# Kernel optimization log

Measured on AMD Instinct MI355X. Metric: run time of the kernel, lower is better.

## Reference

```python
import jax, jax.numpy as jnp
import numpy as np

FACTOR = 5

def setup_inputs() -> dict:
    key = jax.random.key(0)
    kq, kk, kv, ki = jax.random.split(key, 4)
    B, L, H, D = 8, 2048, 8, 64
    u = FACTOR * int(np.ceil(np.log(L)))  # sample_k == n_top == 40
    return {
        "queries": jax.random.normal(kq, (B, L, H, D), dtype=jnp.float32),
        "keys": jax.random.normal(kk, (B, L, H, D), dtype=jnp.float32),
        "values": jax.random.normal(kv, (B, L, H, D), dtype=jnp.float32),
        "index_sample": jax.random.randint(ki, (L, u), 0, L, dtype=jnp.int32),
    }

def reference(queries, keys, values, index_sample):
    B, L, H, D = queries.shape
    # faithful to torch .view(B, H, -1, D) on contiguous tensors (a reshape, not a transpose)
    q = queries.reshape(B, H, L, D)
    k = keys.reshape(B, H, L, D)
    v = values.reshape(B, H, L, D)
    u = FACTOR * int(np.ceil(np.log(L)))  # U_part == u
    # --- _prob_QK: sample keys per query, score, pick top-u queries ---
    K_sample = k[:, :, index_sample, :]                      # [B,H,L,u,D] gather over L_K
    QK_sample = jnp.einsum('bhld,bhlsd->bhls', q, K_sample)  # [B,H,L,u]
    M = QK_sample.max(axis=-1) - QK_sample.sum(axis=-1) / L  # sparsity measure [B,H,L]
    M_top = jax.lax.top_k(M, u)[1]                           # [B,H,u] indices of active queries
    Q_reduce = jnp.take_along_axis(q, M_top[..., None], axis=2)  # [B,H,u,D]
    scores = jnp.einsum('bhud,bhld->bhul', Q_reduce, k)      # [B,H,u,L]
    scale = 1.0 / float(np.sqrt(D))
    attn = jax.nn.softmax(scores * scale, axis=-1)           # dropout is identity in eval
    context = jnp.einsum('bhul,bhld->bhud', attn, v)         # [B,H,u,D]
    return context, attn
```

## Files before the change

### kernel.cpp

```cpp
#include <hip/hip_runtime.h>
#include <math.h>

#define LSEQ 2048
#define DDIM 64
#define UU   40
#define NBH  64
#define NCHUNK 8
#define CROWS  256
#define CTX_ELEMS (NBH*UU*DDIM)

__device__ __forceinline__ float grp8_sum(float x) {
  float t;
  t = __int_as_float(__builtin_amdgcn_update_dpp(0, __float_as_int(x), 0xB1, 0xF, 0xF, false));
  x += t;
  t = __int_as_float(__builtin_amdgcn_update_dpp(0, __float_as_int(x), 0x4E, 0xF, 0xF, false));
  x += t;
  t = __int_as_float(__builtin_amdgcn_update_dpp(0, __float_as_int(x), 0x141, 0xF, 0xF, false));
  x += t;
  return x;
}

__global__ __launch_bounds__(256) void k0_sort(
    const int* __restrict__ idxs, int* __restrict__ sidx, int* __restrict__ soff) {
  int l = blockIdx.x * 4 + (threadIdx.x >> 6);
  int lane = threadIdx.x & 63;
  int v = 0, c = NCHUNK;
  if (lane < UU) { v = idxs[l * UU + lane]; c = v >> 8; }
  unsigned long long lower = (1ull << lane) - 1ull;
  int base = 0;
#pragma unroll
  for (int cc = 0; cc < NCHUNK; ++cc) {
    unsigned long long m = __ballot(c == cc);
    if (c == cc) {
      int rank = __popcll(m & lower);
      sidx[l * UU + base + rank] = v;
    }
    int cnt = __popcll(m);
    if (lane == cc) soff[l * NCHUNK + cc] = (base << 8) | cnt;
    base += cnt;
  }
}

__global__ __launch_bounds__(512, 4) void k12_gather(
    const float* __restrict__ q, const float* __restrict__ k,
    const int* __restrict__ sidx, const int* __restrict__ soff,
    float2* __restrict__ Mpart) {
  __shared__ float4 kt[CROWS * 16];
  int b = blockIdx.x;
  int bh = b & 63;
  int c  = b >> 6;
  int t  = threadIdx.x;

  {
    const float4* src = (const float4*)(k + ((size_t)bh * LSEQ + c * CROWS) * DDIM);
#pragma unroll
    for (int j = 0; j < 8; ++j) {
      int i = t + 512 * j;
      int row = i >> 4, col = i & 15;
      kt[row * 16 + (col ^ (row & 7))] = src[i];
    }
  }
  __syncthreads();

  int w = t >> 6;
  int lane = t & 63;
  int g = lane >> 3;
  int sub = lane & 7;

  for (int lb = 0; lb < 256; lb += 8) {
    int l = w * 256 + lb + g;
    const float4* qr = (const float4*)(q + ((size_t)bh * LSEQ + l) * DDIM);
    float4 qa = qr[sub];
    float4 qb = qr[sub + 8];
    int oc   = soff[l * NCHUNK + c];
    int cnt  = oc & 255;
    int base = oc >> 8;
    int rowv[8];
#pragma unroll
    for (int s = 0; s < 8; ++s) {
      int ix = base + s; ix = ix < UU ? ix : UU - 1;
      rowv[s] = sidx[l * UU + ix] & (CROWS - 1);
    }
    float mx = -INFINITY, sm = 0.f;
#pragma unroll
    for (int s = 0; s < 8; ++s) {
      if (s < cnt) {
        int row = rowv[s];
        int sl = (sub ^ (row & 7));
        float4 a  = kt[row * 16 + sl];
        float4 bq = kt[row * 16 + 8 + sl];
        float d = qa.x * a.x + qa.y * a.y + qa.z * a.z + qa.w * a.w
                + qb.x * bq.x + qb.y * bq.y + qb.z * bq.z + qb.w * bq.w;
        d = grp8_sum(d);
        mx = fmaxf(mx, d);
        sm += d;
      }
    }
    for (int s = 8; s < cnt; ++s) {
      int row = sidx[l * UU + base + s] & (CROWS - 1);
      int sl = (sub ^ (row & 7));
      float4 a  = kt[row * 16 + sl];
      float4 bq = kt[row * 16 + 8 + sl];
      float d = qa.x * a.x + qa.y * a.y + qa.z * a.z + qa.w * a.w
              + qb.x * bq.x + qb.y * bq.y + qb.z * bq.z + qb.w * bq.w;
      d = grp8_sum(d);
      mx = fmaxf(mx, d);
      sm += d;
    }
    if (sub == 0) Mpart[((size_t)bh * NCHUNK + c) * LSEQ + l] = make_float2(mx, sm);
  }
}

__global__ __launch_bounds__(256) void k3_topk(const float2* __restrict__ Mp,
                                               int* __restrict__ Mtop) {
  int bh = blockIdx.x;
  int t = threadIdx.x;
  int w = t >> 6;
  int lane = t & 63;
  float v[8];
#pragma unroll
  for (int j = 0; j < 8; ++j) {
    int l = t + 256 * j;
    float mxv = -INFINITY, smv = 0.f;
#pragma unroll
    for (int c = 0; c < NCHUNK; ++c) {
      float2 p = Mp[((size_t)bh * NCHUNK + c) * LSEQ + l];
      mxv = fmaxf(mxv, p.x);
      smv += p.y;
    }
    v[j] = mxv - smv * (1.0f / (float)LSEQ);
  }
  __shared__ float swv[4];
  __shared__ int   swi[4];
  __shared__ int   win;
  for (int it = 0; it < UU; ++it) {
    float bv = -INFINITY; int bi = 0x7fffffff;
#pragma unroll
    for (int j = 0; j < 8; ++j) {
      if (v[j] > bv) { bv = v[j]; bi = t + 256 * j; }
    }
#pragma unroll
    for (int off = 32; off > 0; off >>= 1) {
      float ov = __shfl_xor(bv, off, 64);
      int   oi = __shfl_xor(bi, off, 64);
      if (ov > bv || (ov == bv && oi < bi)) { bv = ov; bi = oi; }
    }
    if (lane == 0) { swv[w] = bv; swi[w] = bi; }
    __syncthreads();
    if (t == 0) {
      float fv = swv[0]; int fi = swi[0];
#pragma unroll
      for (int j = 1; j < 4; ++j) {
        if (swv[j] > fv || (swv[j] == fv && swi[j] < fi)) { fv = swv[j]; fi = swi[j]; }
      }
      Mtop[bh * UU + it] = fi;
      win = fi;
    }
    __syncthreads();
    int wi = win;
#pragma unroll
    for (int j = 0; j < 8; ++j)
      if (wi == t + 256 * j) v[j] = -INFINITY;
  }
}

__global__ __launch_bounds__(256, 3) void k457_fused(
    const float* __restrict__ q, const float* __restrict__ k,
    const float* __restrict__ v, const int* __restrict__ Mtop,
    float* __restrict__ attn, float* __restrict__ ctx) {
  __shared__ float  sct[4 * LSEQ];
  __shared__ float4 vt4[64 * 16];
  int b = blockIdx.x;
  int bh = b & 63;
  int u0 = (b >> 6) * 4;
  int t = threadIdx.x;

  {
    int g = t >> 2;
    int sub = t & 3;
    float4 qv[4][4];
#pragma unroll
    for (int u = 0; u < 4; ++u) {
      int qi = Mtop[bh * UU + u0 + u];
      const float4* qr = (const float4*)(q + (size_t)(bh * LSEQ + qi) * DDIM);
#pragma unroll
      for (int m = 0; m < 4; ++m) qv[u][m] = qr[4 * m + sub];
    }
    const float* kb = k + (size_t)bh * LSEQ * DDIM;
#pragma unroll 1
    for (int p = 0; p < 32; ++p) {
      int l = p * 64 + g;
      const float4* kr = (const float4*)(kb + (size_t)l * DDIM);
      float4 ks[4];
#pragma unroll
      for (int m = 0; m < 4; ++m) ks[m] = kr[4 * m + sub];
      float d[4];
#pragma unroll
      for (int u = 0; u < 4; ++u) {
        float s = 0.f;
#pragma unroll
        for (int m = 0; m < 4; ++m) {
          float4 x = qv[u][m], a = ks[m];
          s += x.x * a.x + x.y * a.y + x.z * a.z + x.w * a.w;
        }
        s += __shfl_xor(s, 1, 64);
        s += __shfl_xor(s, 2, 64);
        d[u] = s * 0.125f;
      }
      if (sub == 0) {
#pragma unroll
        for (int u = 0; u < 4; ++u) sct[u * LSEQ + l] = d[u];
      }
    }
  }
  __syncthreads();

  int w = t >> 6, lane = t & 63;
  {
    float* row = sct + w * LSEQ;
    float vv[32];
    float mx = -INFINITY;
#pragma unroll
    for (int j = 0; j < 32; ++j) { vv[j] = row[lane + 64 * j]; mx = fmaxf(mx, vv[j]); }
#pragma unroll
    for (int off = 32; off > 0; off >>= 1) mx = fmaxf(mx, __shfl_xor(mx, off, 64));
    float sm = 0.f;
#pragma unroll
    for (int j = 0; j < 32; ++j) { vv[j] = __expf(vv[j] - mx); sm += vv[j]; }
#pragma unroll
    for (int off = 32; off > 0; off >>= 1) sm += __shfl_xor(sm, off, 64);
    float inv = 1.0f / sm;
    float* ap = attn + (size_t)(bh * UU + u0 + w) * LSEQ;
#pragma unroll
    for (int j = 0; j < 32; ++j) {
      float a = vv[j] * inv;
      row[lane + 64 * j] = a;
      ap[lane + 64 * j] = a;
    }
  }
  __syncthreads();

  int dq = lane & 15;
  int lq = lane >> 4;
  float4 acc[4];
#pragma unroll
  for (int u = 0; u < 4; ++u) acc[u] = make_float4(0.f, 0.f, 0.f, 0.f);

  const float4* vsrc = (const float4*)(v + (size_t)bh * LSEQ * DDIM);
#pragma unroll 1
  for (int tile = 0; tile < 32; ++tile) {
#pragma unroll
    for (int i = 0; i < 4; ++i) {
      int idx = t + 256 * i;
      int row = idx >> 4, c4 = idx & 15;
      vt4[row * 16 + (c4 ^ (row & 3))] = vsrc[tile * 1024 + idx];
    }
    __syncthreads();
#pragma unroll
    for (int i = 0; i < 4; ++i) {
      int r = w * 16 + i * 4 + lq;
      int l = tile * 64 + r;
      float4 vv4 = vt4[r * 16 + (dq ^ (r & 3))];
#pragma unroll
      for (int u = 0; u < 4; ++u) {
        float a = sct[u * LSEQ + l];
        acc[u].x += a * vv4.x;
        acc[u].y += a * vv4.y;
        acc[u].z += a * vv4.z;
        acc[u].w += a * vv4.w;
      }
    }
    __syncthreads();
  }

#pragma unroll
  for (int u = 0; u < 4; ++u) {
    acc[u].x += __shfl_xor(acc[u].x, 16, 64);
    acc[u].y += __shfl_xor(acc[u].y, 16, 64);
    acc[u].z += __shfl_xor(acc[u].z, 16, 64);
    acc[u].w += __shfl_xor(acc[u].w, 16, 64);
    acc[u].x += __shfl_xor(acc[u].x, 32, 64);
    acc[u].y += __shfl_xor(acc[u].y, 32, 64);
    acc[u].z += __shfl_xor(acc[u].z, 32, 64);
    acc[u].w += __shfl_xor(acc[u].w, 32, 64);
  }
  __syncthreads();
  float* pacc = (float*)vt4;
  if (lq == 0) {
#pragma unroll
    for (int u = 0; u < 4; ++u)
      ((float4*)pacc)[(w * 4 + u) * 16 + dq] = acc[u];
  }
  __syncthreads();
  {
    int uu = t >> 6, d = t & 63;
    float s = pacc[(0 * 4 + uu) * 64 + d] + pacc[(1 * 4 + uu) * 64 + d]
            + pacc[(2 * 4 + uu) * 64 + d] + pacc[(3 * 4 + uu) * 64 + d];
    ctx[((size_t)bh * UU + u0 + uu) * DDIM + d] = s;
  }
}

extern "C" void kernel_launch(void* const* d_in, const int* in_sizes, int n_in,
                              void* d_out, int out_size, void* d_ws, size_t ws_size,
                              hipStream_t stream) {
  const float* q   = (const float*)d_in[0];
  const float* k   = (const float*)d_in[1];
  const float* v   = (const float*)d_in[2];
  const int*   idx = (const int*)d_in[3];

  float* ctx  = (float*)d_out;
  float* attn = (float*)d_out + CTX_ELEMS;
  float2* Mpart = (float2*)attn;

  int* sidx = (int*)d_ws;
  int* soff = sidx + LSEQ * UU;
  int* Mtop = soff + LSEQ * NCHUNK;

  k0_sort<<<LSEQ / 4, 256, 0, stream>>>(idx, sidx, soff);
  k12_gather<<<NBH * NCHUNK, 512, 0, stream>>>(q, k, sidx, soff, Mpart);
  k3_topk<<<NBH, 256, 0, stream>>>(Mpart, Mtop);
  k457_fused<<<NBH * 10, 256, 0, stream>>>(q, k, v, Mtop, attn, ctx);
}
```

Before: 290.5 us.

## Split key staging into 16 chunks of 128 rows with higher occupancy

Key rows for the sampled-score gather are now staged per block in 16 chunks of 128 rows instead of 8 chunks of 256. This halves shared memory per block, doubles the block count, and raises the occupancy hint. The XOR swizzle on the shared-memory tile is removed and plain contiguous copies are used. Loop iterations that no lane in a wave needs are skipped wave-uniformly, and the index-clamp logic is replaced by padding the workspace so reads past the end stay in bounds. In exchange, the top-k kernel has twice as many partial max/sum pairs to combine, and unswizzled shared reads may cause bank conflicts.

```diff
diff --git a/kernel.cpp b/kernel.cpp
--- a/kernel.cpp
+++ b/kernel.cpp
@@ -5,8 +5,8 @@
 #define DDIM 64
 #define UU   40
 #define NBH  64
-#define NCHUNK 8
-#define CROWS  256
+#define NCHUNK 16
+#define CROWS  128
 #define CTX_ELEMS (NBH*UU*DDIM)
 
 __device__ __forceinline__ float grp8_sum(float x) {
@@ -25,7 +25,7 @@
   int l = blockIdx.x * 4 + (threadIdx.x >> 6);
   int lane = threadIdx.x & 63;
   int v = 0, c = NCHUNK;
-  if (lane < UU) { v = idxs[l * UU + lane]; c = v >> 8; }
+  if (lane < UU) { v = idxs[l * UU + lane]; c = v >> 7; }
   unsigned long long lower = (1ull << lane) - 1ull;
   int base = 0;
 #pragma unroll
@@ -41,7 +41,7 @@
   }
 }
 
-__global__ __launch_bounds__(512, 4) void k12_gather(
+__global__ __launch_bounds__(512, 8) void k12_gather(
     const float* __restrict__ q, const float* __restrict__ k,
     const int* __restrict__ sidx, const int* __restrict__ soff,
     float2* __restrict__ Mpart) {
@@ -54,11 +54,7 @@
   {
     const float4* src = (const float4*)(k + ((size_t)bh * LSEQ + c * CROWS) * DDIM);
 #pragma unroll
-    for (int j = 0; j < 8; ++j) {
-      int i = t + 512 * j;
-      int row = i >> 4, col = i & 15;
-      kt[row * 16 + (col ^ (row & 7))] = src[i];
-    }
+    for (int j = 0; j < 4; ++j) kt[t + 512 * j] = src[t + 512 * j];
   }
   __syncthreads();
 
@@ -67,6 +63,7 @@
   int g = lane >> 3;
   int sub = lane & 7;
 
+#pragma unroll 1
   for (int lb = 0; lb < 256; lb += 8) {
     int l = w * 256 + lb + g;
     const float4* qr = (const float4*)(q + ((size_t)bh * LSEQ + l) * DDIM);
@@ -75,32 +72,31 @@
     int oc   = soff[l * NCHUNK + c];
     int cnt  = oc & 255;
     int base = oc >> 8;
+    const int* sp = sidx + l * UU + base;
     int rowv[8];
 #pragma unroll
+    for (int s = 0; s < 8; ++s) rowv[s] = sp[s] & (CROWS - 1);
+    float mx = -INFINITY, sm = 0.f;
+#pragma unroll
     for (int s = 0; s < 8; ++s) {
-      int ix = base + s; ix = ix < UU ? ix : UU - 1;
-      rowv[s] = sidx[l * UU + ix] & (CROWS - 1);
-    }
-    float mx = -INFINITY, sm = 0.f;
-#pragma unroll
-    for (int s = 0; s < 8; ++s) {
-      if (s < cnt) {
-        int row = rowv[s];
-        int sl = (sub ^ (row & 7));
-        float4 a  = kt[row * 16 + sl];
-        float4 bq = kt[row * 16 + 8 + sl];
-        float d = qa.x * a.x + qa.y * a.y + qa.z * a.z + qa.w * a.w
-                + qb.x * bq.x + qb.y * bq.y + qb.z * bq.z + qb.w * bq.w;
-        d = grp8_sum(d);
-        mx = fmaxf(mx, d);
-        sm += d;
+      if (s == 0 || __any(s < cnt)) {
+        if (s < cnt) {
+          const float4* kr = kt + rowv[s] * 16;
+          float4 a  = kr[sub];
+          float4 bq = kr[sub + 8];
+          float d = qa.x * a.x + qa.y * a.y + qa.z * a.z + qa.w * a.w
+                  + qb.x * bq.x + qb.y * bq.y + qb.z * bq.z + qb.w * bq.w;
+          d = grp8_sum(d);
+          mx = fmaxf(mx, d);
+          sm += d;
+        }
       }
     }
     for (int s = 8; s < cnt; ++s) {
-      int row = sidx[l * UU + base + s] & (CROWS - 1);
-      int sl = (sub ^ (row & 7));
-      float4 a  = kt[row * 16 + sl];
-      float4 bq = kt[row * 16 + 8 + sl];
+      int row = sp[s] & (CROWS - 1);
+      const float4* kr = kt + row * 16;
+      float4 a  = kr[sub];
+      float4 bq = kr[sub + 8];
       float d = qa.x * a.x + qa.y * a.y + qa.z * a.z + qa.w * a.w
               + qb.x * bq.x + qb.y * bq.y + qb.z * bq.z + qb.w * bq.w;
       d = grp8_sum(d);
@@ -313,7 +309,7 @@
   float2* Mpart = (float2*)attn;
 
   int* sidx = (int*)d_ws;
-  int* soff = sidx + LSEQ * UU;
+  int* soff = sidx + LSEQ * UU + 16;
   int* Mtop = soff + LSEQ * NCHUNK;
 
   k0_sort<<<LSEQ / 4, 256, 0, stream>>>(idx, sidx, soff);
```

Result: no change. 293.1 us (+0.9%).
